# Kernel tuning notes

Hardware: AMD Instinct MI355X
Metric: run time of the kernel (lower is better)

The kernel has to match this reference:

```python
import jax, jax.numpy as jnp
import numpy as np

EPS = 1e-5  # torch LayerNorm default


def _lstm_layer(x, Wih, Whh, bih, bhh):
    """Batched multi-weight LSTM layer.
    x: (N, T, I); Wih: (N, 4H, I); Whh: (N, 4H, H); bih, bhh: (N, 4H).
    Gate order matches PyTorch: i, f, g, o.
    Returns (hs: (N, T, H), h_last: (N, H)).
    """
    N, T, _ = x.shape
    H = Whh.shape[-1]
    # Precompute input projections for all timesteps (high-intensity GEMM).
    xW = jnp.einsum('nti,ngi->ntg', x, Wih) + (bih + bhh)[:, None, :]  # (N, T, 4H)

    def step(carry, xt):
        h, c = carry
        gates = xt + jnp.einsum('nh,ngh->ng', h, Whh)  # (N, 4H)
        i, f, g, o = jnp.split(gates, 4, axis=-1)
        i = jax.nn.sigmoid(i)
        f = jax.nn.sigmoid(f)
        g = jnp.tanh(g)
        o = jax.nn.sigmoid(o)
        c = f * c + i * g
        h = o * jnp.tanh(c)
        return (h, c), h

    h0 = jnp.zeros((N, H), dtype=x.dtype)
    c0 = jnp.zeros((N, H), dtype=x.dtype)
    (h_last, _), hs = jax.lax.scan(step, (h0, c0), jnp.swapaxes(xW, 0, 1))
    return jnp.swapaxes(hs, 0, 1), h_last


def _layer_norm(x, gamma, beta):
    mu = jnp.mean(x, axis=-1, keepdims=True)
    var = jnp.mean(jnp.square(x - mu), axis=-1, keepdims=True)
    return (x - mu) * jax.lax.rsqrt(var + EPS) * gamma + beta


def setup_inputs() -> dict:
    key = jax.random.key(0)
    N, T, I, H = 128, 512, 32, 256
    ks = jax.random.split(key, 10)
    k = 1.0 / np.sqrt(H)  # torch LSTM init scale
    u = lambda kk, shape: jax.random.uniform(kk, shape, jnp.float32, -k, k)
    return {
        'x': jax.random.normal(ks[0], (N, T, I), jnp.float32),
        # layer 0 (input I -> H)
        'Wih0': u(ks[1], (N, 4 * H, I)),
        'Whh0': u(ks[2], (N, 4 * H, H)),
        'bih0': u(ks[3], (N, 4 * H)),
        'bhh0': u(ks[4], (N, 4 * H)),
        # layer 1 (H -> H)
        'Wih1': u(ks[5], (N, 4 * H, H)),
        'Whh1': u(ks[6], (N, 4 * H, H)),
        'bih1': u(ks[7], (N, 4 * H)),
        'bhh1': u(ks[8], (N, 4 * H)),
        # LayerNorm params
        'gamma': jnp.ones((H,), jnp.float32),
        'beta': jnp.zeros((H,), jnp.float32),
    }


def reference(x, Wih0, Whh0, bih0, bhh0, Wih1, Whh1, bih1, bhh1, gamma, beta):
    # Eval-mode forward: Dropout layers are identity.
    hs0, _ = _lstm_layer(x, Wih0, Whh0, bih0, bhh0)      # (N, T, H)
    _, h_last = _lstm_layer(hs0, Wih1, Whh1, bih1, bhh1)  # (N, H) = top-layer final hidden state
    return _layer_norm(h_last, gamma, beta)               # (N, H)
```

## Files before the change

### kernel.cpp

```cpp
#include <hip/hip_runtime.h>
#include <hip/hip_bf16.h>


typedef _Float16 half2_t __attribute__((ext_vector_type(2)));
typedef _Float16 half8_t __attribute__((ext_vector_type(8)));
typedef float floatx4 __attribute__((ext_vector_type(4)));

__device__ __forceinline__ unsigned pk(float a, float b) {
  half2_t h = { (_Float16)a, (_Float16)b };
  return __builtin_bit_cast(unsigned, h);
}
__device__ __forceinline__ float fdot2(unsigned w, unsigned h, float c) {
  return __builtin_amdgcn_fdot2(__builtin_bit_cast(half2_t, w),
                                __builtin_bit_cast(half2_t, h), c, false);
}
__device__ __forceinline__ float h2f(unsigned short u) {
  return (float)__builtin_bit_cast(_Float16, u);
}
__device__ __forceinline__ unsigned short f2h(float f) {
  return __builtin_bit_cast(unsigned short, (_Float16)f);
}
__device__ __forceinline__ float sigmf(float x) {
  return __builtin_amdgcn_rcpf(1.f + __expf(-x));
}
__device__ __forceinline__ float tanh_(float x) {
  return 2.f * sigmf(2.f * x) - 1.f;
}
__device__ __forceinline__ floatx4 mfma16(half8_t a, half8_t b, floatx4 c) {
  return __builtin_amdgcn_mfma_f32_16x16x32_f16(a, b, c, 0, 0, 0);
}
__device__ __forceinline__ unsigned rlane(unsigned v, int l) {
  return (unsigned)__builtin_amdgcn_readlane((int)v, l);
}

template<int K, int KT, bool AF16>
__global__ __launch_bounds__(256)
void gemm_xw(const void* __restrict__ Ap, const float* __restrict__ Bp,
             unsigned short* __restrict__ Cp)
{
  __shared__ unsigned short As[128][KT + 8];
  __shared__ unsigned short Bs[128][KT + 8];
  const int tid = threadIdx.x;
  const int node = blockIdx.y;
  const int mt = blockIdx.x >> 3;
  const int nt = blockIdx.x & 7;
  const int lane = tid & 63, wv = tid >> 6;
  const int wr = wv >> 1, wc = wv & 1;
  const int lm = lane & 15, lk = (lane >> 4) * 8;

  floatx4 zero = {0.f, 0.f, 0.f, 0.f};
  floatx4 acc[4][4];
#pragma unroll
  for (int i = 0; i < 4; ++i)
#pragma unroll
    for (int j = 0; j < 4; ++j) acc[i][j] = zero;

  for (int kt = 0; kt < K; kt += KT) {
    if (AF16) {
      const unsigned short* A = (const unsigned short*)Ap + (size_t)node * 512 * K;
      const int CPR = KT / 8;
#pragma unroll
      for (int c = tid; c < 128 * CPR; c += 256) {
        int r = c / CPR, cc = (c % CPR) * 8;
        *(uint4*)&As[r][cc] =
            *(const uint4*)(A + (size_t)(mt * 128 + r) * K + kt + cc);
      }
    } else {
      const float* A = (const float*)Ap + (size_t)node * 512 * K;
      const int CPR = KT / 4;
#pragma unroll
      for (int c = tid; c < 128 * CPR; c += 256) {
        int r = c / CPR, cc = (c % CPR) * 4;
        float4 v = *(const float4*)(A + (size_t)(mt * 128 + r) * K + kt + cc);
        uint2 p = make_uint2(pk(v.x, v.y), pk(v.z, v.w));
        *(uint2*)&As[r][cc] = p;
      }
    }
    {
      const float* B = Bp + (size_t)node * 1024 * K;
      const int CPR = KT / 4;
#pragma unroll
      for (int c = tid; c < 128 * CPR; c += 256) {
        int r = c / CPR, cc = (c % CPR) * 4;
        float4 v = *(const float4*)(B + (size_t)(nt * 128 + r) * K + kt + cc);
        uint2 p = make_uint2(pk(v.x, v.y), pk(v.z, v.w));
        *(uint2*)&Bs[r][cc] = p;
      }
    }
    __syncthreads();
#pragma unroll
    for (int ks = 0; ks < KT / 32; ++ks) {
      half8_t af[4], bf[4];
#pragma unroll
      for (int i = 0; i < 4; ++i)
        af[i] = *(const half8_t*)&As[wr * 64 + i * 16 + lm][ks * 32 + lk];
#pragma unroll
      for (int j = 0; j < 4; ++j)
        bf[j] = *(const half8_t*)&Bs[wc * 64 + j * 16 + lm][ks * 32 + lk];
#pragma unroll
      for (int i = 0; i < 4; ++i)
#pragma unroll
        for (int j = 0; j < 4; ++j)
          acc[i][j] = mfma16(af[i], bf[j], acc[i][j]);
    }
    __syncthreads();
  }
  unsigned short* C = Cp + (size_t)node * 512 * 1024;
#pragma unroll
  for (int i = 0; i < 4; ++i)
#pragma unroll
    for (int j = 0; j < 4; ++j)
#pragma unroll
      for (int r = 0; r < 4; ++r) {
        int row = mt * 128 + wr * 64 + i * 16 + (lane >> 4) * 4 + r;
        int col = nt * 128 + wc * 64 + j * 16 + lm;
        C[(size_t)row * 1024 + col] = f2h(acc[i][j][r]);
      }
}

#define VWP 96

template<bool WRITE_HS, bool FINAL>
__global__ __launch_bounds__(512, 2)
void lstm_rec(const unsigned short* __restrict__ xW,
              const float* __restrict__ Whh,
              const float* __restrict__ bih, const float* __restrict__ bhh,
              unsigned* __restrict__ hs,
              const float* __restrict__ gamma, const float* __restrict__ beta,
              float* __restrict__ out)
{
  __shared__ uint4 lw4[16][512];
  __shared__ __align__(16) unsigned short hbuf[256];
  __shared__ float fBuf[256], oBuf[256];
  __shared__ float redBuf[2];

  const int tid = threadIdx.x;
  const int lane = tid & 63;
  const int n = blockIdx.x;
  const int g0 = tid, g1 = tid + 512;

  const float b0 = bih[n * 1024 + g0] + bhh[n * 1024 + g0];
  const float b1 = bih[n * 1024 + g1] + bhh[n * 1024 + g1];

  const float4* w0p = (const float4*)(Whh + ((size_t)n * 1024 + g0) * 256);
  const float4* w1p = (const float4*)(Whh + ((size_t)n * 1024 + g1) * 256);
  unsigned wv0[VWP], wv1[VWP];
#pragma unroll
  for (int i = 0; i < VWP / 2; ++i) {
    float4 v = w0p[i];
    wv0[2 * i] = pk(v.x, v.y);
    wv0[2 * i + 1] = pk(v.z, v.w);
    float4 u = w1p[i];
    wv1[2 * i] = pk(u.x, u.y);
    wv1[2 * i + 1] = pk(u.z, u.w);
  }
#pragma unroll
  for (int i = 0; i < 8; ++i) {
    float4 a = w0p[48 + 2 * i], b = w0p[49 + 2 * i];
    lw4[i][tid] = make_uint4(pk(a.x, a.y), pk(a.z, a.w), pk(b.x, b.y), pk(b.z, b.w));
    float4 c4 = w1p[48 + 2 * i], d4 = w1p[49 + 2 * i];
    lw4[8 + i][tid] = make_uint4(pk(c4.x, c4.y), pk(c4.z, c4.w), pk(d4.x, d4.y), pk(d4.z, d4.w));
  }

  if (tid < 32) ((uint4*)hbuf)[tid] = make_uint4(0, 0, 0, 0);
  float c = 0.f, hl = 0.f;
  const unsigned short* xwp = xW + (size_t)n * 512 * 1024;
  __syncthreads();

  for (int t = 0; t < 512; ++t) {
    unsigned short xu0 = xwp[t * 1024 + g0];
    unsigned short xu1 = xwp[t * 1024 + g1];
    float a0 = b0, a1 = b1;
    const uint2 hv = ((const uint2*)hbuf)[lane];
#pragma unroll
    for (int q = 0; q < 24; ++q) {
      const unsigned s0 = rlane(hv.x, 2 * q);
      const unsigned s1 = rlane(hv.y, 2 * q);
      const unsigned s2 = rlane(hv.x, 2 * q + 1);
      const unsigned s3 = rlane(hv.y, 2 * q + 1);
      a0 = fdot2(wv0[4 * q + 0], s0, a0); a1 = fdot2(wv1[4 * q + 0], s0, a1);
      a0 = fdot2(wv0[4 * q + 1], s1, a0); a1 = fdot2(wv1[4 * q + 1], s1, a1);
      a0 = fdot2(wv0[4 * q + 2], s2, a0); a1 = fdot2(wv1[4 * q + 2], s2, a1);
      a0 = fdot2(wv0[4 * q + 3], s3, a0); a1 = fdot2(wv1[4 * q + 3], s3, a1);
    }
#pragma unroll
    for (int q = 0; q < 8; ++q) {
      uint4 u0 = lw4[q][tid], u1 = lw4[8 + q][tid];
      const int l0 = 48 + 2 * q;
      const unsigned s0 = rlane(hv.x, l0);
      const unsigned s1 = rlane(hv.y, l0);
      const unsigned s2 = rlane(hv.x, l0 + 1);
      const unsigned s3 = rlane(hv.y, l0 + 1);
      a0 = fdot2(u0.x, s0, a0); a1 = fdot2(u1.x, s0, a1);
      a0 = fdot2(u0.y, s1, a0); a1 = fdot2(u1.y, s1, a1);
      a0 = fdot2(u0.z, s2, a0); a1 = fdot2(u1.z, s2, a1);
      a0 = fdot2(u0.w, s3, a0); a1 = fdot2(u1.w, s3, a1);
    }
    a0 += h2f(xu0);
    a1 += h2f(xu1);

    float iact = 0.f, gact = 0.f;
    if (tid < 256) {
      iact = sigmf(a0);
      gact = tanh_(a1);
    } else {
      fBuf[tid - 256] = sigmf(a0);
      oBuf[tid - 256] = sigmf(a1);
    }
    __syncthreads();
    if (tid < 256) {
      c = fBuf[tid] * c + iact * gact;
      hl = oBuf[tid] * tanh_(c);
      hbuf[tid] = f2h(hl);
    }
    __syncthreads();
    if (WRITE_HS && tid < 128)
      hs[((size_t)n * 512 + t) * 128 + tid] = ((const unsigned*)hbuf)[tid];
  }

  if (FINAL) {
    if (tid < 256) fBuf[tid] = hl;
    __syncthreads();
    if (tid < 64) {
      float s = fBuf[tid] + fBuf[tid + 64] + fBuf[tid + 128] + fBuf[tid + 192];
      for (int off = 32; off > 0; off >>= 1) s += __shfl_down(s, off, 64);
      if (tid == 0) redBuf[0] = s * (1.f / 256.f);
    }
    __syncthreads();
    float mu = redBuf[0];
    if (tid < 256) oBuf[tid] = (hl - mu) * (hl - mu);
    __syncthreads();
    if (tid < 64) {
      float s = oBuf[tid] + oBuf[tid + 64] + oBuf[tid + 128] + oBuf[tid + 192];
      for (int off = 32; off > 0; off >>= 1) s += __shfl_down(s, off, 64);
      if (tid == 0) redBuf[1] = s * (1.f / 256.f);
    }
    __syncthreads();
    if (tid < 256) {
      float var = redBuf[1];
      out[(size_t)n * 256 + tid] =
          (hl - mu) * rsqrtf(var + 1e-5f) * gamma[tid] + beta[tid];
    }
  }
}

extern "C" void kernel_launch(void* const* d_in, const int* in_sizes, int n_in,
                              void* d_out, int out_size, void* d_ws, size_t ws_size,
                              hipStream_t stream) {
  const float* x     = (const float*)d_in[0];
  const float* Wih0  = (const float*)d_in[1];
  const float* Whh0  = (const float*)d_in[2];
  const float* bih0  = (const float*)d_in[3];
  const float* bhh0  = (const float*)d_in[4];
  const float* Wih1  = (const float*)d_in[5];
  const float* Whh1  = (const float*)d_in[6];
  const float* bih1  = (const float*)d_in[7];
  const float* bhh1  = (const float*)d_in[8];
  const float* gamma = (const float*)d_in[9];
  const float* beta  = (const float*)d_in[10];
  float* out = (float*)d_out;

  unsigned short* xw  = (unsigned short*)d_ws;
  unsigned short* hs0 = (unsigned short*)((char*)d_ws + (size_t)134217728);

  gemm_xw<32, 32, false><<<dim3(32, 128), 256, 0, stream>>>(x, Wih0, xw);
  lstm_rec<true, false><<<128, 512, 0, stream>>>(xw, Whh0, bih0, bhh0,
                                                 (unsigned*)hs0, nullptr, nullptr,
                                                 nullptr);
  gemm_xw<256, 128, true><<<dim3(32, 128), 256, 0, stream>>>(hs0, Wih1, xw);
  lstm_rec<false, true><<<128, 512, 0, stream>>>(xw, Whh1, bih1, bhh1, nullptr,
                                                 gamma, beta, out);
}
```

Baseline: 2.437 ms.

## Remap LSTM gates per wave, exchange via shuffles, double-buffer hidden state

Gate rows are reassigned so that each wave holds i/g gates in its low half-lanes and f/o gates for the same hidden units in its high half-lanes. The gate exchange then happens through __shfl_xor instead of shared memory, which removes one of the two per-step __syncthreads. The hidden-state buffer is double-buffered so the remaining barrier is enough, the next step's xW values are prefetched, and the dot products are split across two accumulators to shorten the dependency chain. tanh for g is computed as 2*sigmoid(2x)-1. Half of each wave's lanes sit idle during the cell update.

```diff
diff --git a/kernel.cpp b/kernel.cpp
--- a/kernel.cpp
+++ b/kernel.cpp
@@ -130,14 +130,19 @@
               float* __restrict__ out)
 {
   __shared__ uint4 lw4[16][512];
-  __shared__ __align__(16) unsigned short hbuf[256];
-  __shared__ float fBuf[256], oBuf[256];
+  __shared__ __align__(16) unsigned short hbuf[2][256];
+  __shared__ float fLN[256], sLN[256];
   __shared__ float redBuf[2];
 
   const int tid = threadIdx.x;
   const int lane = tid & 63;
+  const int w = tid >> 6;
   const int n = blockIdx.x;
-  const int g0 = tid, g1 = tid + 512;
+  const int lo = lane & 31;
+  const bool lowHalf = lane < 32;
+  const int d = w * 32 + lo;
+  const int g0 = lowHalf ? d : 256 + d;
+  const int g1 = lowHalf ? 512 + d : 768 + d;
 
   const float b0 = bih[n * 1024 + g0] + bhh[n * 1024 + g0];
   const float b1 = bih[n * 1024 + g1] + bhh[n * 1024 + g1];
@@ -162,26 +167,28 @@
     lw4[8 + i][tid] = make_uint4(pk(c4.x, c4.y), pk(c4.z, c4.w), pk(d4.x, d4.y), pk(d4.z, d4.w));
   }
 
-  if (tid < 32) ((uint4*)hbuf)[tid] = make_uint4(0, 0, 0, 0);
+  if (tid < 32) ((uint4*)hbuf[0])[tid] = make_uint4(0, 0, 0, 0);
   float c = 0.f, hl = 0.f;
   const unsigned short* xwp = xW + (size_t)n * 512 * 1024;
+  unsigned short xu0 = xwp[g0], xu1 = xwp[g1];
   __syncthreads();
 
   for (int t = 0; t < 512; ++t) {
-    unsigned short xu0 = xwp[t * 1024 + g0];
-    unsigned short xu1 = xwp[t * 1024 + g1];
-    float a0 = b0, a1 = b1;
-    const uint2 hv = ((const uint2*)hbuf)[lane];
+    const uint2 hv = ((const uint2*)hbuf[t & 1])[lane];
+    const unsigned short* xn = xwp + (size_t)((t + 1) & 511) * 1024;
+    const unsigned short nxu0 = xn[g0], nxu1 = xn[g1];
+
+    float aA0 = b0, aB0 = 0.f, aA1 = b1, aB1 = 0.f;
 #pragma unroll
     for (int q = 0; q < 24; ++q) {
       const unsigned s0 = rlane(hv.x, 2 * q);
       const unsigned s1 = rlane(hv.y, 2 * q);
       const unsigned s2 = rlane(hv.x, 2 * q + 1);
       const unsigned s3 = rlane(hv.y, 2 * q + 1);
-      a0 = fdot2(wv0[4 * q + 0], s0, a0); a1 = fdot2(wv1[4 * q + 0], s0, a1);
-      a0 = fdot2(wv0[4 * q + 1], s1, a0); a1 = fdot2(wv1[4 * q + 1], s1, a1);
-      a0 = fdot2(wv0[4 * q + 2], s2, a0); a1 = fdot2(wv1[4 * q + 2], s2, a1);
-      a0 = fdot2(wv0[4 * q + 3], s3, a0); a1 = fdot2(wv1[4 * q + 3], s3, a1);
+      aA0 = fdot2(wv0[4 * q + 0], s0, aA0); aA1 = fdot2(wv1[4 * q + 0], s0, aA1);
+      aB0 = fdot2(wv0[4 * q + 1], s1, aB0); aB1 = fdot2(wv1[4 * q + 1], s1, aB1);
+      aA0 = fdot2(wv0[4 * q + 2], s2, aA0); aA1 = fdot2(wv1[4 * q + 2], s2, aA1);
+      aB0 = fdot2(wv0[4 * q + 3], s3, aB0); aB1 = fdot2(wv1[4 * q + 3], s3, aB1);
     }
 #pragma unroll
     for (int q = 0; q < 8; ++q) {
@@ -191,55 +198,55 @@
       const unsigned s1 = rlane(hv.y, l0);
       const unsigned s2 = rlane(hv.x, l0 + 1);
       const unsigned s3 = rlane(hv.y, l0 + 1);
-      a0 = fdot2(u0.x, s0, a0); a1 = fdot2(u1.x, s0, a1);
-      a0 = fdot2(u0.y, s1, a0); a1 = fdot2(u1.y, s1, a1);
-      a0 = fdot2(u0.z, s2, a0); a1 = fdot2(u1.z, s2, a1);
-      a0 = fdot2(u0.w, s3, a0); a1 = fdot2(u1.w, s3, a1);
-    }
-    a0 += h2f(xu0);
-    a1 += h2f(xu1);
-
-    float iact = 0.f, gact = 0.f;
-    if (tid < 256) {
-      iact = sigmf(a0);
-      gact = tanh_(a1);
-    } else {
-      fBuf[tid - 256] = sigmf(a0);
-      oBuf[tid - 256] = sigmf(a1);
-    }
-    __syncthreads();
-    if (tid < 256) {
-      c = fBuf[tid] * c + iact * gact;
-      hl = oBuf[tid] * tanh_(c);
-      hbuf[tid] = f2h(hl);
+      aA0 = fdot2(u0.x, s0, aA0); aA1 = fdot2(u1.x, s0, aA1);
+      aB0 = fdot2(u0.y, s1, aB0); aB1 = fdot2(u1.y, s1, aB1);
+      aA0 = fdot2(u0.z, s2, aA0); aA1 = fdot2(u1.z, s2, aA1);
+      aB0 = fdot2(u0.w, s3, aB0); aB1 = fdot2(u1.w, s3, aB1);
+    }
+    float a0 = (aA0 + aB0) + h2f(xu0);
+    float a1 = (aA1 + aB1) + h2f(xu1);
+    xu0 = nxu0; xu1 = nxu1;
+
+    const float act0 = sigmf(a0);
+    const float r1 = sigmf(lowHalf ? 2.f * a1 : a1);
+    const float act1 = lowHalf ? 2.f * r1 - 1.f : r1;
+    const float p0 = __shfl_xor(act0, 32, 64);
+    const float p1 = __shfl_xor(act1, 32, 64);
+    if (lowHalf) {
+      c = p0 * c + act0 * act1;
+      hl = p1 * tanh_(c);
+      hbuf[(t + 1) & 1][d] = f2h(hl);
     }
     __syncthreads();
     if (WRITE_HS && tid < 128)
-      hs[((size_t)n * 512 + t) * 128 + tid] = ((const unsigned*)hbuf)[tid];
+      hs[((size_t)n * 512 + t) * 128 + tid] = ((const unsigned*)hbuf[(t + 1) & 1])[tid];
   }
 
   if (FINAL) {
-    if (tid < 256) fBuf[tid] = hl;
+    if (lowHalf) fLN[d] = hl;
     __syncthreads();
     if (tid < 64) {
-      float s = fBuf[tid] + fBuf[tid + 64] + fBuf[tid + 128] + fBuf[tid + 192];
+      float s = fLN[tid] + fLN[tid + 64] + fLN[tid + 128] + fLN[tid + 192];
       for (int off = 32; off > 0; off >>= 1) s += __shfl_down(s, off, 64);
       if (tid == 0) redBuf[0] = s * (1.f / 256.f);
     }
     __syncthreads();
-    float mu = redBuf[0];
-    if (tid < 256) oBuf[tid] = (hl - mu) * (hl - mu);
+    const float mu = redBuf[0];
+    if (tid < 256) {
+      const float dv = fLN[tid] - mu;
+      sLN[tid] = dv * dv;
+    }
     __syncthreads();
     if (tid < 64) {
-      float s = oBuf[tid] + oBuf[tid + 64] + oBuf[tid + 128] + oBuf[tid + 192];
+      float s = sLN[tid] + sLN[tid + 64] + sLN[tid + 128] + sLN[tid + 192];
       for (int off = 32; off > 0; off >>= 1) s += __shfl_down(s, off, 64);
       if (tid == 0) redBuf[1] = s * (1.f / 256.f);
     }
     __syncthreads();
     if (tid < 256) {
-      float var = redBuf[1];
+      const float var = redBuf[1];
       out[(size_t)n * 256 + tid] =
-          (hl - mu) * rsqrtf(var + 1e-5f) * gamma[tid] + beta[tid];
+          (fLN[tid] - mu) * rsqrtf(var + 1e-5f) * gamma[tid] + beta[tid];
     }
   }
 }
```

Result: no change. 2.442 ms (+0.2%).
